# Kernel tuning notes

Hardware: AMD Instinct MI355X
Metric: run time of the kernel (lower is better)

The kernel has to match this reference:

```python
import jax, jax.numpy as jnp
import numpy as np

N = 16384       # number of points (single graph; batch all zeros)
DIN = 3         # input_dim
DOUT = 3        # output_dim
H = 16          # hidden_dim
K = 16          # k nearest neighbors
L = 4           # n_edgeconvs


def setup_inputs() -> dict:
    key = jax.random.key(0)
    ks = jax.random.split(key, 6)
    def w(k, shape, fan_in):
        return jax.random.normal(k, shape, jnp.float32) / np.float32(np.sqrt(fan_in))
    return {
        "x":     jax.random.normal(ks[0], (N, DIN), jnp.float32),
        "emb_W": w(ks[1], (DIN, H), DIN),
        "emb_b": jnp.zeros((H,), jnp.float32),
        "ec_W1": w(ks[2], (L, 2 * H, H), 2 * H),
        "ec_b1": jnp.zeros((L, H), jnp.float32),
        "ec_W2": w(ks[3], (L, H, H), H),
        "ec_b2": jnp.zeros((L, H), jnp.float32),
        "out_W": w(ks[4], (L * H, DOUT), L * H),
        "out_b": jnp.zeros((DOUT,), jnp.float32),
    }


def knn_idx(x, k):
    """Indices [N, k] of k nearest neighbors (no self-loops), like torch_cluster.knn_graph."""
    x = jax.lax.stop_gradient(x)  # graph construction is non-differentiable
    sq = jnp.sum(x * x, axis=-1)
    d = sq[:, None] + sq[None, :] - 2.0 * (x @ x.T)  # [N, N] squared distances
    n = x.shape[0]
    d = d.at[jnp.arange(n), jnp.arange(n)].set(jnp.inf)  # exclude self
    _, idx = jax.lax.top_k(-d, k)
    return idx  # idx[i] = k nearest neighbors j of center i


def edgeconv(x, idx, W1, b1, W2, b2):
    """EdgeConv with aggr='mean': mean_j MLP([x_i, x_j - x_i])."""
    nbr = x[idx]                                      # [N, K, H] gather
    ctr = jnp.broadcast_to(x[:, None, :], nbr.shape)  # [N, K, H]
    feat = jnp.concatenate([ctr, nbr - ctr], axis=-1) # [N, K, 2H]
    msg = jax.nn.relu(feat @ W1 + b1) @ W2 + b2       # [N, K, H]
    return jnp.mean(msg, axis=1)                      # exact k-regular scatter-mean


def reference(x, emb_W, emb_b, ec_W1, ec_b1, ec_W2, ec_b2, out_W, out_b):
    h = jax.nn.relu(x @ emb_W + emb_b)  # embedding
    outs = []
    for l in range(L):  # small fixed layer loop
        idx = knn_idx(h, K)  # kNN graph rebuilt on current features each layer
        h = edgeconv(h, idx, ec_W1[l], ec_b1[l], ec_W2[l], ec_b2[l])
        outs.append(h)
    return jnp.concatenate(outs, axis=-1) @ out_W + out_b  # [N, DOUT]
```

## Files before the change

### kernel.cpp

```cpp
#include <hip/hip_runtime.h>
#include <hip/hip_bf16.h>

#define GN 16384
#define GH 16
#define GK 16
#define GL 4
#define HPS 20

#define RPB 32
#define NTHR 1024
#define CAP 160
#define BSTR 161
#define SSTR 264
#define TILE_C 256
#define TILE_F (TILE_C*HPS)
#define LDS_TILE (2*RPB*BSTR + 2*RPB)
#define LDS_TOT  (LDS_TILE + TILE_F)

#define INFF __builtin_inff()

#define OFF_H     0
#define OFF_IDX   (5*GN*HPS)
#define OFF_FLAGS (OFF_IDX + GN*GK)
#define OFF_XF    (OFF_FLAGS + GN)
#define OFF_EMBW  (OFF_XF + GN*3)
#define OFF_EMBB  (OFF_EMBW + 3*GH)
#define OFF_W1    (OFF_EMBB + GH)
#define OFF_B1    (OFF_W1 + GL*2*GH*GH)
#define OFF_W2    (OFF_B1 + GL*GH)
#define OFF_B2    (OFF_W2 + GL*GH*GH)
#define OFF_OW    (OFF_B2 + GL*GH)
#define OFF_OB    (OFF_OW + GL*GH*3)
#define OFF_DFLAG (OFF_OB + 4)

__global__ void detect_kernel(const unsigned short* __restrict__ raw,
                              int* __restrict__ flag)
{
    if (threadIdx.x == 0 && blockIdx.x == 0) {
        int cnt = 0;
        for (int i = 0; i < 64; ++i) {
            unsigned int bits = ((unsigned int)raw[2*i]) << 16;
            float v = __uint_as_float(bits);
            float a = fabsf(v);
            if (a > 1e-4f && a < 50.f) ++cnt;
        }
        *flag = (cnt >= 32) ? 1 : 0;
    }
}

__global__ void convert_kernel(const void* __restrict__ src,
                               float* __restrict__ dst, int n,
                               const int* __restrict__ flag)
{
    int i = blockIdx.x * 256 + threadIdx.x;
    if (i >= n) return;
    if (*flag)
        dst[i] = __bfloat162float(((const __hip_bfloat16*)src)[i]);
    else
        dst[i] = ((const float*)src)[i];
}

__device__ __forceinline__ float distt(const float hi[16], float sqi,
                                       const float* __restrict__ hj)
{
    float4 A = *(const float4*)(hj + 0);
    float4 B = *(const float4*)(hj + 4);
    float4 C = *(const float4*)(hj + 8);
    float4 D = *(const float4*)(hj + 12);
    float sqj = hj[16];
    float d0 = hi[0]*A.x;
    float d1 = hi[1]*A.y;
    d0 = fmaf(hi[2],  A.z, d0);  d1 = fmaf(hi[3],  A.w, d1);
    d0 = fmaf(hi[4],  B.x, d0);  d1 = fmaf(hi[5],  B.y, d1);
    d0 = fmaf(hi[6],  B.z, d0);  d1 = fmaf(hi[7],  B.w, d1);
    d0 = fmaf(hi[8],  C.x, d0);  d1 = fmaf(hi[9],  C.y, d1);
    d0 = fmaf(hi[10], C.z, d0);  d1 = fmaf(hi[11], C.w, d1);
    d0 = fmaf(hi[12], D.x, d0);  d1 = fmaf(hi[13], D.y, d1);
    d0 = fmaf(hi[14], D.z, d0);  d1 = fmaf(hi[15], D.w, d1);
    return fmaf(-2.f, d0 + d1, sqi + sqj);
}

#define LOAD_HI(ptr)                                                        \
    float hi[16]; float sqi;                                                \
    {                                                                       \
        const float* _hr = (ptr);                                           \
        float4 A = *(const float4*)(_hr + 0);                               \
        float4 B = *(const float4*)(_hr + 4);                               \
        float4 C = *(const float4*)(_hr + 8);                               \
        float4 D = *(const float4*)(_hr + 12);                              \
        hi[0]=A.x; hi[1]=A.y; hi[2]=A.z; hi[3]=A.w;                         \
        hi[4]=B.x; hi[5]=B.y; hi[6]=B.z; hi[7]=B.w;                         \
        hi[8]=C.x; hi[9]=C.y; hi[10]=C.z; hi[11]=C.w;                       \
        hi[12]=D.x; hi[13]=D.y; hi[14]=D.z; hi[15]=D.w;                     \
        sqi = _hr[16];                                                      \
    }

__global__ __launch_bounds__(256) void embed_kernel(
    const float* __restrict__ xf, const float* __restrict__ W,
    const float* __restrict__ b, float* __restrict__ h0)
{
    int i = blockIdx.x * 256 + threadIdx.x;
    float x0 = xf[i*3+0], x1 = xf[i*3+1], x2 = xf[i*3+2];
    float* orow = h0 + i * HPS;
    float sq = 0.f;
#pragma unroll
    for (int c = 0; c < GH; ++c) {
        float t = b[c];
        t = fmaf(x0, W[0*GH+c], t);
        t = fmaf(x1, W[1*GH+c], t);
        t = fmaf(x2, W[2*GH+c], t);
        t = fmaxf(t, 0.f);
        orow[c] = t;
        sq = fmaf(t, t, sq);
    }
    orow[16] = sq;
}

__global__ __launch_bounds__(NTHR, 4) void knn4_kernel(
    const float* __restrict__ hp, int* __restrict__ idxout,
    int* __restrict__ flags)
{
    __shared__ float lds[LDS_TOT];
    float*    bufd = lds;
    int*      bufj = (int*)(lds + RPB*BSTR);
    unsigned* cnt  = (unsigned*)(lds + 2*RPB*BSTR);
    float*    tau  = lds + 2*RPB*BSTR + RPB;
    float*    tile = lds + LDS_TILE;
    float4*   tile4 = (float4*)tile;

    const int tid = threadIdx.x;
    const int q   = tid & 7;
    const int s   = tid >> 3;
    const int r0  = blockIdx.x * RPB + q * 4;

    float hi[4][16]; float sqi[4];
#pragma unroll
    for (int rr = 0; rr < 4; ++rr) {
        const float* hr = hp + (r0 + rr) * HPS;
        float4 A = *(const float4*)(hr + 0);
        float4 B = *(const float4*)(hr + 4);
        float4 C = *(const float4*)(hr + 8);
        float4 D = *(const float4*)(hr + 12);
        hi[rr][0]=A.x; hi[rr][1]=A.y; hi[rr][2]=A.z; hi[rr][3]=A.w;
        hi[rr][4]=B.x; hi[rr][5]=B.y; hi[rr][6]=B.z; hi[rr][7]=B.w;
        hi[rr][8]=C.x; hi[rr][9]=C.y; hi[rr][10]=C.z; hi[rr][11]=C.w;
        hi[rr][12]=D.x; hi[rr][13]=D.y; hi[rr][14]=D.z; hi[rr][15]=D.w;
        sqi[rr] = hr[16];
    }

    const int c0 = tid / 5, f0 = tid - 5*c0;
    const bool has2 = tid < (TILE_C*5 - NTHR);
    const int v1 = tid + NTHR;
    const int c1 = v1 / 5, f1 = v1 - 5*c1;
    const float4* hp4 = (const float4*)hp;
    const int o1a = 20*c0 + f0, o1b = 20*c1 + f1;
    const int o2a = 5*c0 + f0,  o2b = 5*c1 + f1;

#define DIST4(hjp, jglob, dd)                                               \
    {                                                                       \
        const float* _hj = (hjp);                                           \
        float4 A = *(const float4*)(_hj + 0);                               \
        float4 B = *(const float4*)(_hj + 4);                               \
        float4 C = *(const float4*)(_hj + 8);                               \
        float4 D = *(const float4*)(_hj + 12);                              \
        float sqj = _hj[16];                                                \
        _Pragma("unroll")                                                   \
        for (int rr = 0; rr < 4; ++rr) {                                    \
            float d0 = hi[rr][0]*A.x;                                       \
            float d1 = hi[rr][1]*A.y;                                       \
            d0 = fmaf(hi[rr][2],  A.z, d0);  d1 = fmaf(hi[rr][3],  A.w, d1);\
            d0 = fmaf(hi[rr][4],  B.x, d0);  d1 = fmaf(hi[rr][5],  B.y, d1);\
            d0 = fmaf(hi[rr][6],  B.z, d0);  d1 = fmaf(hi[rr][7],  B.w, d1);\
            d0 = fmaf(hi[rr][8],  C.x, d0);  d1 = fmaf(hi[rr][9],  C.y, d1);\
            d0 = fmaf(hi[rr][10], C.z, d0);  d1 = fmaf(hi[rr][11], C.w, d1);\
            d0 = fmaf(hi[rr][12], D.x, d0);  d1 = fmaf(hi[rr][13], D.y, d1);\
            d0 = fmaf(hi[rr][14], D.z, d0);  d1 = fmaf(hi[rr][15], D.w, d1);\
            dd[rr] = fmaf(-2.f, d0 + d1, sqi[rr] + sqj);                    \
        }                                                                   \
        unsigned u = (unsigned)((jglob) - r0);                              \
        if (u < 4u) {                                                       \
            _Pragma("unroll")                                               \
            for (int rr = 0; rr < 4; ++rr)                                  \
                if (u == (unsigned)rr) dd[rr] = INFF;                       \
        }                                                                   \
    }

    float m1[4], m2[4];
#pragma unroll
    for (int rr = 0; rr < 4; ++rr) { m1[rr] = INFF; m2[rr] = INFF; }
    {
        float4 ga, gb;
        ga = hp4[o1a];
        if (has2) gb = hp4[o1b];
        for (int k = 0; k < 16; ++k) {
            __syncthreads();
            tile4[tid] = ga;
            if (has2) tile4[v1] = gb;
            if (k + 1 < 16) {
                ga = hp4[5120*(k+1) + o1a];
                if (has2) gb = hp4[5120*(k+1) + o1b];
            }
            __syncthreads();
#pragma unroll
            for (int cc = 0; cc < 2; ++cc) {
                const int lc = s + cc*128;
                const int j = 4*(256*k + lc);
                float dd[4];
                DIST4(tile + lc*HPS, j, dd);
#pragma unroll
                for (int rr = 0; rr < 4; ++rr) {
                    float t = fmaxf(m1[rr], dd[rr]);
                    m1[rr] = fminf(m1[rr], dd[rr]);
                    m2[rr] = fminf(m2[rr], t);
                }
            }
        }
    }
#pragma unroll
    for (int rr = 0; rr < 4; ++rr) {
        lds[(q*4+rr)*SSTR + s*2 + 0] = m1[rr];
        lds[(q*4+rr)*SSTR + s*2 + 1] = m2[rr];
    }
    __syncthreads();

    const int mr = tid >> 5, g = tid & 31;
    float s8[8];
    {
        float4 u0 = *(const float4*)(lds + mr*SSTR + g*8);
        float4 u1 = *(const float4*)(lds + mr*SSTR + g*8 + 4);
        s8[0]=u0.x; s8[1]=u0.y; s8[2]=u0.z; s8[3]=u0.w;
        s8[4]=u1.x; s8[5]=u1.y; s8[6]=u1.z; s8[7]=u1.w;
    }
    float tval = INFF;
#pragma unroll
    for (int k = 0; k < 16; ++k) {
        float md = s8[0]; int ms = 0;
#pragma unroll
        for (int e = 1; e < 8; ++e) { bool cs = (s8[e] < md); md = cs ? s8[e] : md; ms = cs ? e : ms; }
        float rv = md; int rl = g;
#pragma unroll
        for (int m = 1; m <= 16; m <<= 1) {
            float ov = __shfl_xor(rv, m, 32);
            int   ol = __shfl_xor(rl, m, 32);
            bool cs = (ov < rv) || (ov == rv && ol < rl);
            rv = cs ? ov : rv; rl = cs ? ol : rl;
        }
        if (rl == g) {
#pragma unroll
            for (int e = 0; e < 8; ++e) if (e == ms) s8[e] = INFF;
        }
        tval = rv;
    }
    if (g == 0) tau[mr] = tval;
    if (tid < RPB) cnt[tid] = 0;
    __syncthreads();

    float tau4[4];
#pragma unroll
    for (int rr = 0; rr < 4; ++rr) tau4[rr] = tau[q*4+rr];
    {
        float4 ga, gb;
        ga = hp4[o2a];
        if (has2) gb = hp4[o2b];
        for (int k = 0; k < GN/TILE_C; ++k) {
            __syncthreads();
            tile4[tid] = ga;
            if (has2) tile4[v1] = gb;
            if (k + 1 < GN/TILE_C) {
                ga = hp4[1280*(k+1) + o2a];
                if (has2) gb = hp4[1280*(k+1) + o2b];
            }
            __syncthreads();
#pragma unroll
            for (int cc = 0; cc < 2; ++cc) {
                const int lc = s + cc*128;
                const int j = 256*k + lc;
                float dd[4];
                DIST4(tile + lc*HPS, j, dd);
                bool p0 = dd[0] <= tau4[0], p1 = dd[1] <= tau4[1];
                bool p2 = dd[2] <= tau4[2], p3 = dd[3] <= tau4[3];
                if (p0 | p1 | p2 | p3) {
#pragma unroll
                    for (int rr = 0; rr < 4; ++rr) {
                        if (dd[rr] <= tau4[rr]) {
                            unsigned pos = atomicAdd(&cnt[q*4+rr], 1u);
                            if (pos < CAP) {
                                bufd[(q*4+rr)*BSTR + pos] = dd[rr];
                                bufj[(q*4+rr)*BSTR + pos] = j;
                            }
                        }
                    }
                }
            }
        }
    }
    __syncthreads();

    const unsigned c   = cnt[mr];
    const unsigned lim = c < CAP ? c : CAP;
    float sd[5]; int sj[5];
#pragma unroll
    for (int e = 0; e < 5; ++e) {
        unsigned p = (unsigned)g + 32u*e;
        bool v = p < lim;
        sd[e] = v ? bufd[mr*BSTR + p] : INFF;
        sj[e] = v ? bufj[mr*BSTR + p] : 0x7fffffff;
    }
    const int rowg = blockIdx.x * RPB + mr;
#pragma unroll
    for (int k = 0; k < GK; ++k) {
        float md = sd[0]; int mj = sj[0]; int ms = 0;
#pragma unroll
        for (int e = 1; e < 5; ++e) {
            bool cs = (sd[e] < md) || (sd[e] == md && sj[e] < mj);
            md = cs ? sd[e] : md; mj = cs ? sj[e] : mj; ms = cs ? e : ms;
        }
        float rd = md; int rj = mj;
#pragma unroll
        for (int m = 1; m <= 16; m <<= 1) {
            float od = __shfl_xor(rd, m, 32);
            int   oj = __shfl_xor(rj, m, 32);
            bool cs = (od < rd) || (od == rd && oj < rj);
            rd = cs ? od : rd; rj = cs ? oj : rj;
        }
        if (g == 0) idxout[rowg*GK + k] = rj;
        if (rd == md && rj == mj) {
#pragma unroll
            for (int e = 0; e < 5; ++e) if (e == ms) { sd[e] = INFF; sj[e] = 0x7fffffff; }
        }
    }
    if (g == 0) flags[rowg] = (c > CAP || c < 16u) ? 1 : 0;
#undef DIST4
}

__global__ __launch_bounds__(64) void rescue_kernel(
    const float* __restrict__ hp, const int* __restrict__ flags,
    int* __restrict__ idxout)
{
    const int lane = threadIdx.x;
    const int r0 = blockIdx.x * RPB;
    int f = (lane < RPB) ? flags[r0 + lane] : 0;
    if (__ballot(f != 0) == 0ull) return;
    for (int rr = 0; rr < RPB; ++rr) {
        if (flags[r0 + rr] == 0) continue;
        const int row = r0 + rr;
        LOAD_HI(hp + row * HPS);
        float topd[GK]; int topi[GK];
#pragma unroll
        for (int s = 0; s < GK; ++s) { topd[s] = INFF; topi[s] = -1; }
        float mx = INFF; int mxs = 0;
        for (int s = 0; s < GN/64; ++s) {
            int j = lane + (s << 6);
            float d = distt(hi, sqi, hp + j * HPS);
            if (j == row) d = INFF;
            if (d < mx) {
#pragma unroll
                for (int e = 0; e < GK; ++e) { bool cs = (e == mxs); topd[e] = cs ? d : topd[e]; topi[e] = cs ? j : topi[e]; }
                mx = topd[0]; mxs = 0;
#pragma unroll
                for (int e = 1; e < GK; ++e) { bool cs = (topd[e] >= mx); mx = cs ? topd[e] : mx; mxs = cs ? e : mxs; }
            }
        }
#pragma unroll
        for (int t = 0; t < GK; ++t) {
            float md = topd[0]; int mj = topi[0]; int ms = 0;
#pragma unroll
            for (int e = 1; e < GK; ++e) {
                bool cs = (topd[e] < md) || (topd[e] == md && topi[e] < mj);
                md = cs ? topd[e] : md; mj = cs ? topi[e] : mj; ms = cs ? e : ms;
            }
            float rd = md; int rj = mj;
#pragma unroll
            for (int m = 1; m <= 32; m <<= 1) {
                float od = __shfl_xor(rd, m, 64);
                int   oj = __shfl_xor(rj, m, 64);
                bool cs = (od < rd) || (od == rd && oj < rj);
                rd = cs ? od : rd; rj = cs ? oj : rj;
            }
            if (lane == 0) idxout[row*GK + t] = rj;
            if (rd == md && rj == mj) {
#pragma unroll
                for (int e = 0; e < GK; ++e) if (e == ms) { topd[e] = INFF; topi[e] = 0x7fffffff; }
            }
        }
    }
}

__global__ __launch_bounds__(256) void edgeconv_kernel(
    const float* __restrict__ hin, const int* __restrict__ idx,
    const float* __restrict__ W1, const float* __restrict__ b1,
    const float* __restrict__ W2, const float* __restrict__ b2,
    float* __restrict__ hout)
{
    __shared__ float sW1[2*GH*GH], sW2[GH*GH], sb1[GH], sb2[GH];
    const int tid = threadIdx.x;
    for (int t = tid; t < 2*GH*GH; t += 256) sW1[t] = W1[t];
    for (int t = tid; t < GH*GH;  t += 256) sW2[t] = W2[t];
    if (tid < GH) { sb1[tid] = b1[tid]; sb2[tid] = b2[tid]; }
    __syncthreads();

    const int t4 = tid & 3;
    const int i = blockIdx.x * 64 + (tid >> 2);

    LOAD_HI(hin + i * HPS);
    (void)sqi;
    float ci[GH];
#pragma unroll
    for (int c = 0; c < GH; ++c) {
        float s = sb1[c];
#pragma unroll
        for (int d = 0; d < GH; ++d) s = fmaf(hi[d], sW1[d*GH+c], s);
        ci[c] = s;
    }
    float acc[GH];
#pragma unroll
    for (int c = 0; c < GH; ++c) acc[c] = 0.f;

    const int4 jj = *(const int4*)(idx + i*GK + t4*4);
    const int js[4] = { jj.x, jj.y, jj.z, jj.w };
#pragma unroll
    for (int nn = 0; nn < 4; ++nn) {
        const int j = js[nn];
        float dj[GH];
        {
            const float* hv = hin + j * HPS;
            float4 A = *(const float4*)(hv + 0);
            float4 B = *(const float4*)(hv + 4);
            float4 C = *(const float4*)(hv + 8);
            float4 D = *(const float4*)(hv + 12);
            dj[0]=A.x-hi[0]; dj[1]=A.y-hi[1]; dj[2]=A.z-hi[2]; dj[3]=A.w-hi[3];
            dj[4]=B.x-hi[4]; dj[5]=B.y-hi[5]; dj[6]=B.z-hi[6]; dj[7]=B.w-hi[7];
            dj[8]=C.x-hi[8]; dj[9]=C.y-hi[9]; dj[10]=C.z-hi[10]; dj[11]=C.w-hi[11];
            dj[12]=D.x-hi[12]; dj[13]=D.y-hi[13]; dj[14]=D.z-hi[14]; dj[15]=D.w-hi[15];
        }
        float msg[GH];
#pragma unroll
        for (int c = 0; c < GH; ++c) {
            float s = ci[c];
#pragma unroll
            for (int d = 0; d < GH; ++d) s = fmaf(dj[d], sW1[(GH+d)*GH+c], s);
            msg[c] = fmaxf(s, 0.f);
        }
#pragma unroll
        for (int c2 = 0; c2 < GH; ++c2) {
            float s = acc[c2];
#pragma unroll
            for (int c = 0; c < GH; ++c) s = fmaf(msg[c], sW2[c*GH+c2], s);
            acc[c2] = s;
        }
    }
#pragma unroll
    for (int c = 0; c < GH; ++c) {
        acc[c] += __shfl_xor(acc[c], 1);
        acc[c] += __shfl_xor(acc[c], 2);
    }
    if (t4 == 0) {
        float* orow = hout + i * HPS;
        float sq = 0.f;
#pragma unroll
        for (int c = 0; c < GH; ++c) {
            float v = acc[c] * (1.f/16.f) + sb2[c];
            orow[c] = v;
            sq = fmaf(v, v, sq);
        }
        orow[16] = sq;
    }
}

__global__ __launch_bounds__(256) void out_kernel(
    const float* __restrict__ hbase, const float* __restrict__ W,
    const float* __restrict__ b, void* __restrict__ out,
    const int* __restrict__ flag)
{
    int i = blockIdx.x * 256 + threadIdx.x;
    float a0 = b[0], a1 = b[1], a2 = b[2];
#pragma unroll
    for (int l = 0; l < GL; ++l) {
        const float* hp = hbase + l * GN * HPS + i * HPS;
#pragma unroll
        for (int c = 0; c < GH; ++c) {
            const float v = hp[c];
            const float* wr = W + (l * GH + c) * 3;
            a0 = fmaf(v, wr[0], a0);
            a1 = fmaf(v, wr[1], a1);
            a2 = fmaf(v, wr[2], a2);
        }
    }
    if (*flag) {
        __hip_bfloat16* o = (__hip_bfloat16*)out;
        o[i*3+0] = __float2bfloat16(a0);
        o[i*3+1] = __float2bfloat16(a1);
        o[i*3+2] = __float2bfloat16(a2);
    } else {
        float* o = (float*)out;
        o[i*3+0] = a0; o[i*3+1] = a1; o[i*3+2] = a2;
    }
}

extern "C" void kernel_launch(void* const* d_in, const int* in_sizes, int n_in,
                              void* d_out, int out_size, void* d_ws, size_t ws_size,
                              hipStream_t stream)
{
    float* wsf  = (float*)d_ws;
    int* idxb   = (int*)(wsf + OFF_IDX);
    int* flagsb = (int*)(wsf + OFF_FLAGS);
    int* dflag  = (int*)(wsf + OFF_DFLAG);

    detect_kernel<<<1, 64, 0, stream>>>((const unsigned short*)d_in[0], dflag);

    const int segoff[9] = {OFF_XF, OFF_EMBW, OFF_EMBB, OFF_W1, OFF_B1,
                           OFF_W2, OFF_B2, OFF_OW, OFF_OB};
    const int segn[9]   = {GN*3, 3*GH, GH, GL*2*GH*GH, GL*GH,
                           GL*GH*GH, GL*GH, GL*GH*3, 3};
    for (int s = 0; s < 9; ++s)
        convert_kernel<<<(segn[s] + 255)/256, 256, 0, stream>>>(
            d_in[s], wsf + segoff[s], segn[s], dflag);

    embed_kernel<<<GN/256, 256, 0, stream>>>(
        wsf + OFF_XF, wsf + OFF_EMBW, wsf + OFF_EMBB, wsf + OFF_H);

    for (int l = 0; l < GL; ++l) {
        const float* hin = wsf + OFF_H + l*GN*HPS;
        float* hout      = wsf + OFF_H + (l+1)*GN*HPS;
        knn4_kernel<<<GN/RPB, NTHR, 0, stream>>>(hin, idxb, flagsb);
        rescue_kernel<<<GN/RPB, 64, 0, stream>>>(hin, flagsb, idxb);
        edgeconv_kernel<<<GN/64, 256, 0, stream>>>(hin, idxb,
            wsf + OFF_W1 + l*2*GH*GH, wsf + OFF_B1 + l*GH,
            wsf + OFF_W2 + l*GH*GH,  wsf + OFF_B2 + l*GH, hout);
    }

    out_kernel<<<GN/256, 256, 0, stream>>>(
        wsf + OFF_H + GN*HPS, wsf + OFF_OW, wsf + OFF_OB, d_out, dflag);
}
```

Before: 1.271 ms.

## Shrink kNN blocks to 256 threads and parallelize rescue across warps

The kNN kernel moves from 1024 to 256 threads per block. Each thread now covers 8 candidate columns per tile instead of 2, and the tau selection and final top-k reductions shrink from 32-lane to 8-lane groups with more elements per lane. Register prefetch of the next tile is dropped in favour of plain strided cooperative loads. The rescue kernel now runs 16 warps per block, each handling different flagged rows in parallel instead of one warp looping over all rows. The aim is better occupancy and fewer, cheaper shuffle reductions, at the cost of losing load/compute overlap and holding 20-element register arrays per lane.

```diff
diff --git a/kernel.cpp b/kernel.cpp
--- a/kernel.cpp
+++ b/kernel.cpp
@@ -7,11 +7,11 @@
 #define GL 4
 #define HPS 20
 
+#define TPB 256
 #define RPB 32
-#define NTHR 1024
 #define CAP 160
 #define BSTR 161
-#define SSTR 264
+#define SSTR2 68
 #define TILE_C 256
 #define TILE_F (TILE_C*HPS)
 #define LDS_TILE (2*RPB*BSTR + 2*RPB)
@@ -116,7 +116,7 @@
     orow[16] = sq;
 }
 
-__global__ __launch_bounds__(NTHR, 4) void knn4_kernel(
+__global__ void knn11_kernel(
     const float* __restrict__ hp, int* __restrict__ idxout,
     int* __restrict__ flags)
 {
@@ -127,11 +127,15 @@
     float*    tau  = lds + 2*RPB*BSTR + RPB;
     float*    tile = lds + LDS_TILE;
     float4*   tile4 = (float4*)tile;
+    const float4* hp4 = (const float4*)hp;
 
     const int tid = threadIdx.x;
     const int q   = tid & 7;
     const int s   = tid >> 3;
-    const int r0  = blockIdx.x * RPB + q * 4;
+    const int rb  = blockIdx.x * RPB;
+    const int r0  = rb + q * 4;
+
+    if (tid < RPB) cnt[tid] = 0;
 
     float hi[4][16]; float sqi[4];
 #pragma unroll
@@ -147,14 +151,6 @@
         hi[rr][12]=D.x; hi[rr][13]=D.y; hi[rr][14]=D.z; hi[rr][15]=D.w;
         sqi[rr] = hr[16];
     }
-
-    const int c0 = tid / 5, f0 = tid - 5*c0;
-    const bool has2 = tid < (TILE_C*5 - NTHR);
-    const int v1 = tid + NTHR;
-    const int c1 = v1 / 5, f1 = v1 - 5*c1;
-    const float4* hp4 = (const float4*)hp;
-    const int o1a = 20*c0 + f0, o1b = 20*c1 + f1;
-    const int o2a = 5*c0 + f0,  o2b = 5*c1 + f1;
 
 #define DIST4(hjp, jglob, dd)                                               \
     {                                                                       \
@@ -188,106 +184,90 @@
     float m1[4], m2[4];
 #pragma unroll
     for (int rr = 0; rr < 4; ++rr) { m1[rr] = INFF; m2[rr] = INFF; }
+    for (int t = 0; t < 16; ++t) {
+        __syncthreads();
+        for (int v = tid; v < TILE_C*5; v += TPB) {
+            int c = v / 5, f = v - 5*c;
+            tile4[v] = hp4[20*(t*256 + c) + f];
+        }
+        __syncthreads();
+#pragma unroll 2
+        for (int cc = 0; cc < 8; ++cc) {
+            const int lc = s + 32*cc;
+            const int j = 4*(t*256 + lc);
+            float dd[4];
+            DIST4(tile + lc*HPS, j, dd);
+#pragma unroll
+            for (int rr = 0; rr < 4; ++rr) {
+                float h2 = fmaxf(m1[rr], dd[rr]);
+                m1[rr] = fminf(m1[rr], dd[rr]);
+                m2[rr] = fminf(m2[rr], h2);
+            }
+        }
+    }
+    __syncthreads();
+#pragma unroll
+    for (int rr = 0; rr < 4; ++rr) {
+        lds[(q*4+rr)*SSTR2 + s*2 + 0] = m1[rr];
+        lds[(q*4+rr)*SSTR2 + s*2 + 1] = m2[rr];
+    }
+    __syncthreads();
+
+    const int mr = tid >> 3, g = tid & 7;
     {
-        float4 ga, gb;
-        ga = hp4[o1a];
-        if (has2) gb = hp4[o1b];
+        float sv[8];
+        float4 u0 = *(const float4*)(lds + mr*SSTR2 + g*8);
+        float4 u1 = *(const float4*)(lds + mr*SSTR2 + g*8 + 4);
+        sv[0]=u0.x; sv[1]=u0.y; sv[2]=u0.z; sv[3]=u0.w;
+        sv[4]=u1.x; sv[5]=u1.y; sv[6]=u1.z; sv[7]=u1.w;
+        float tv = INFF;
+#pragma unroll
         for (int k = 0; k < 16; ++k) {
-            __syncthreads();
-            tile4[tid] = ga;
-            if (has2) tile4[v1] = gb;
-            if (k + 1 < 16) {
-                ga = hp4[5120*(k+1) + o1a];
-                if (has2) gb = hp4[5120*(k+1) + o1b];
-            }
-            __syncthreads();
-#pragma unroll
-            for (int cc = 0; cc < 2; ++cc) {
-                const int lc = s + cc*128;
-                const int j = 4*(256*k + lc);
-                float dd[4];
-                DIST4(tile + lc*HPS, j, dd);
+            float md = sv[0]; int ms = 0;
+#pragma unroll
+            for (int e = 1; e < 8; ++e) { bool cs = (sv[e] < md); md = cs ? sv[e] : md; ms = cs ? e : ms; }
+            float rv = md; int rl = g;
+#pragma unroll
+            for (int mm = 1; mm <= 4; mm <<= 1) {
+                float ov = __shfl_xor(rv, mm, 8);
+                int   ol = __shfl_xor(rl, mm, 8);
+                bool cs = (ov < rv) || (ov == rv && ol < rl);
+                rv = cs ? ov : rv; rl = cs ? ol : rl;
+            }
+            tv = rv;
+            if (rl == g) {
+#pragma unroll
+                for (int e = 0; e < 8; ++e) if (e == ms) sv[e] = INFF;
+            }
+        }
+        if (g == 0) tau[mr] = tv;
+    }
+    __syncthreads();
+
+    float tau4[4];
+#pragma unroll
+    for (int rr = 0; rr < 4; ++rr) tau4[rr] = tau[q*4+rr];
+    for (int k = 0; k < GN/TILE_C; ++k) {
+        __syncthreads();
+        for (int v = tid; v < TILE_C*5; v += TPB)
+            tile4[v] = hp4[k*(TILE_C*5) + v];
+        __syncthreads();
+#pragma unroll 2
+        for (int cc = 0; cc < 8; ++cc) {
+            const int lc = s + 32*cc;
+            const int j = k*TILE_C + lc;
+            float dd[4];
+            DIST4(tile + lc*HPS, j, dd);
+            bool p0 = dd[0] <= tau4[0], p1 = dd[1] <= tau4[1];
+            bool p2 = dd[2] <= tau4[2], p3 = dd[3] <= tau4[3];
+            if (p0 | p1 | p2 | p3) {
 #pragma unroll
                 for (int rr = 0; rr < 4; ++rr) {
-                    float t = fmaxf(m1[rr], dd[rr]);
-                    m1[rr] = fminf(m1[rr], dd[rr]);
-                    m2[rr] = fminf(m2[rr], t);
-                }
-            }
-        }
-    }
-#pragma unroll
-    for (int rr = 0; rr < 4; ++rr) {
-        lds[(q*4+rr)*SSTR + s*2 + 0] = m1[rr];
-        lds[(q*4+rr)*SSTR + s*2 + 1] = m2[rr];
-    }
-    __syncthreads();
-
-    const int mr = tid >> 5, g = tid & 31;
-    float s8[8];
-    {
-        float4 u0 = *(const float4*)(lds + mr*SSTR + g*8);
-        float4 u1 = *(const float4*)(lds + mr*SSTR + g*8 + 4);
-        s8[0]=u0.x; s8[1]=u0.y; s8[2]=u0.z; s8[3]=u0.w;
-        s8[4]=u1.x; s8[5]=u1.y; s8[6]=u1.z; s8[7]=u1.w;
-    }
-    float tval = INFF;
-#pragma unroll
-    for (int k = 0; k < 16; ++k) {
-        float md = s8[0]; int ms = 0;
-#pragma unroll
-        for (int e = 1; e < 8; ++e) { bool cs = (s8[e] < md); md = cs ? s8[e] : md; ms = cs ? e : ms; }
-        float rv = md; int rl = g;
-#pragma unroll
-        for (int m = 1; m <= 16; m <<= 1) {
-            float ov = __shfl_xor(rv, m, 32);
-            int   ol = __shfl_xor(rl, m, 32);
-            bool cs = (ov < rv) || (ov == rv && ol < rl);
-            rv = cs ? ov : rv; rl = cs ? ol : rl;
-        }
-        if (rl == g) {
-#pragma unroll
-            for (int e = 0; e < 8; ++e) if (e == ms) s8[e] = INFF;
-        }
-        tval = rv;
-    }
-    if (g == 0) tau[mr] = tval;
-    if (tid < RPB) cnt[tid] = 0;
-    __syncthreads();
-
-    float tau4[4];
-#pragma unroll
-    for (int rr = 0; rr < 4; ++rr) tau4[rr] = tau[q*4+rr];
-    {
-        float4 ga, gb;
-        ga = hp4[o2a];
-        if (has2) gb = hp4[o2b];
-        for (int k = 0; k < GN/TILE_C; ++k) {
-            __syncthreads();
-            tile4[tid] = ga;
-            if (has2) tile4[v1] = gb;
-            if (k + 1 < GN/TILE_C) {
-                ga = hp4[1280*(k+1) + o2a];
-                if (has2) gb = hp4[1280*(k+1) + o2b];
-            }
-            __syncthreads();
-#pragma unroll
-            for (int cc = 0; cc < 2; ++cc) {
-                const int lc = s + cc*128;
-                const int j = 256*k + lc;
-                float dd[4];
-                DIST4(tile + lc*HPS, j, dd);
-                bool p0 = dd[0] <= tau4[0], p1 = dd[1] <= tau4[1];
-                bool p2 = dd[2] <= tau4[2], p3 = dd[3] <= tau4[3];
-                if (p0 | p1 | p2 | p3) {
-#pragma unroll
-                    for (int rr = 0; rr < 4; ++rr) {
-                        if (dd[rr] <= tau4[rr]) {
-                            unsigned pos = atomicAdd(&cnt[q*4+rr], 1u);
-                            if (pos < CAP) {
-                                bufd[(q*4+rr)*BSTR + pos] = dd[rr];
-                                bufj[(q*4+rr)*BSTR + pos] = j;
-                            }
+                    if (dd[rr] <= tau4[rr]) {
+                        unsigned pos = atomicAdd(&cnt[q*4+rr], 1u);
+                        if (pos < CAP) {
+                            bufd[(q*4+rr)*BSTR + pos] = dd[rr];
+                            bufj[(q*4+rr)*BSTR + pos] = j;
                         }
                     }
                 }
@@ -296,52 +276,55 @@
     }
     __syncthreads();
 
-    const unsigned c   = cnt[mr];
-    const unsigned lim = c < CAP ? c : CAP;
-    float sd[5]; int sj[5];
-#pragma unroll
-    for (int e = 0; e < 5; ++e) {
-        unsigned p = (unsigned)g + 32u*e;
-        bool v = p < lim;
-        sd[e] = v ? bufd[mr*BSTR + p] : INFF;
-        sj[e] = v ? bufj[mr*BSTR + p] : 0x7fffffff;
-    }
-    const int rowg = blockIdx.x * RPB + mr;
-#pragma unroll
-    for (int k = 0; k < GK; ++k) {
-        float md = sd[0]; int mj = sj[0]; int ms = 0;
-#pragma unroll
-        for (int e = 1; e < 5; ++e) {
-            bool cs = (sd[e] < md) || (sd[e] == md && sj[e] < mj);
-            md = cs ? sd[e] : md; mj = cs ? sj[e] : mj; ms = cs ? e : ms;
-        }
-        float rd = md; int rj = mj;
-#pragma unroll
-        for (int m = 1; m <= 16; m <<= 1) {
-            float od = __shfl_xor(rd, m, 32);
-            int   oj = __shfl_xor(rj, m, 32);
-            bool cs = (od < rd) || (od == rd && oj < rj);
-            rd = cs ? od : rd; rj = cs ? oj : rj;
-        }
-        if (g == 0) idxout[rowg*GK + k] = rj;
-        if (rd == md && rj == mj) {
-#pragma unroll
-            for (int e = 0; e < 5; ++e) if (e == ms) { sd[e] = INFF; sj[e] = 0x7fffffff; }
-        }
-    }
-    if (g == 0) flags[rowg] = (c > CAP || c < 16u) ? 1 : 0;
+    {
+        const unsigned c2  = cnt[mr];
+        const unsigned lim = c2 < CAP ? c2 : CAP;
+        float sd[20]; int sj[20];
+#pragma unroll
+        for (int e = 0; e < 20; ++e) {
+            unsigned p = (unsigned)g + 8u*e;
+            bool v = p < lim;
+            sd[e] = v ? bufd[mr*BSTR + p] : INFF;
+            sj[e] = v ? bufj[mr*BSTR + p] : 0x7fffffff;
+        }
+        const int rowg = rb + mr;
+#pragma unroll
+        for (int k = 0; k < GK; ++k) {
+            float md = sd[0]; int mj = sj[0]; int ms = 0;
+#pragma unroll
+            for (int e = 1; e < 20; ++e) {
+                bool cs = (sd[e] < md) || (sd[e] == md && sj[e] < mj);
+                md = cs ? sd[e] : md; mj = cs ? sj[e] : mj; ms = cs ? e : ms;
+            }
+            float rd = md; int rj = mj;
+#pragma unroll
+            for (int mm = 1; mm <= 4; mm <<= 1) {
+                float od = __shfl_xor(rd, mm, 8);
+                int   oj = __shfl_xor(rj, mm, 8);
+                bool cs = (od < rd) || (od == rd && oj < rj);
+                rd = cs ? od : rd; rj = cs ? oj : rj;
+            }
+            if (g == 0) idxout[rowg*GK + k] = rj;
+            if (rd == md && rj == mj) {
+#pragma unroll
+                for (int e = 0; e < 20; ++e) if (e == ms) { sd[e] = INFF; sj[e] = 0x7fffffff; }
+            }
+        }
+        if (g == 0) flags[rowg] = (c2 > CAP || c2 < 16u) ? 1 : 0;
+    }
 #undef DIST4
 }
 
-__global__ __launch_bounds__(64) void rescue_kernel(
+__global__ __launch_bounds__(1024) void rescue_kernel(
     const float* __restrict__ hp, const int* __restrict__ flags,
     int* __restrict__ idxout)
 {
-    const int lane = threadIdx.x;
+    const int lane = threadIdx.x & 63;
+    const int ww   = threadIdx.x >> 6;
     const int r0 = blockIdx.x * RPB;
     int f = (lane < RPB) ? flags[r0 + lane] : 0;
     if (__ballot(f != 0) == 0ull) return;
-    for (int rr = 0; rr < RPB; ++rr) {
+    for (int rr = ww; rr < RPB; rr += 16) {
         if (flags[r0 + rr] == 0) continue;
         const int row = r0 + rr;
         LOAD_HI(hp + row * HPS);
@@ -522,8 +505,8 @@
     for (int l = 0; l < GL; ++l) {
         const float* hin = wsf + OFF_H + l*GN*HPS;
         float* hout      = wsf + OFF_H + (l+1)*GN*HPS;
-        knn4_kernel<<<GN/RPB, NTHR, 0, stream>>>(hin, idxb, flagsb);
-        rescue_kernel<<<GN/RPB, 64, 0, stream>>>(hin, flagsb, idxb);
+        knn11_kernel<<<GN/RPB, TPB, 0, stream>>>(hin, idxb, flagsb);
+        rescue_kernel<<<GN/RPB, 1024, 0, stream>>>(hin, flagsb, idxb);
         edgeconv_kernel<<<GN/64, 256, 0, stream>>>(hin, idxb,
             wsf + OFF_W1 + l*2*GH*GH, wsf + OFF_B1 + l*GH,
             wsf + OFF_W2 + l*GH*GH,  wsf + OFF_B2 + l*GH, hout);
```

Result: slower. 1.662 ms (+30.8%).
